# Kernel tuning notes

Hardware: AMD Instinct MI355X
Metric: run time of the kernel (lower is better)

Reference implementation:

```python
import jax, jax.numpy as jnp
import numpy as np

DIM = 128
N_HEADS = 4
HEAD_DIM = DIM // N_HEADS
EPS = 1e-5


def setup_inputs() -> dict:
    key = jax.random.key(0)
    ks = jax.random.split(key, 6)
    B, L, D = 1, 256, DIM
    s = 1.0 / np.sqrt(D)
    return {
        "z": jax.random.normal(ks[0], (B, L, L, D), dtype=jnp.float32),
        "ln_g": jnp.ones((D,), dtype=jnp.float32),
        "ln_b": jnp.zeros((D,), dtype=jnp.float32),
        "w_qkv": jax.random.normal(ks[1], (D, 3 * D), dtype=jnp.float32) * s,
        "b_qkv": jnp.zeros((3 * D,), dtype=jnp.float32),
        "w_proj": jax.random.normal(ks[2], (D, D), dtype=jnp.float32) * s,
        "b_proj": jnp.zeros((D,), dtype=jnp.float32),
    }


def reference(z, ln_g, ln_b, w_qkv, b_qkv, w_proj, b_proj):
    # z: (B, L1, L2, D); axis='row' -> attention along L2 for each (B, L1) row
    B, L1, L2, D = z.shape
    H, hd = N_HEADS, HEAD_DIM

    mu = jnp.mean(z, axis=-1, keepdims=True)
    var = jnp.mean(jnp.square(z - mu), axis=-1, keepdims=True)
    zn = (z - mu) * jax.lax.rsqrt(var + EPS) * ln_g + ln_b

    qkv = zn @ w_qkv + b_qkv                      # (B, L1, L2, 3D)
    qkv = qkv.reshape(B, L1, L2, 3, H, hd)
    q, k, v = qkv[..., 0, :, :], qkv[..., 1, :, :], qkv[..., 2, :, :]  # (B,L1,L2,H,hd)

    scale = 1.0 / jnp.sqrt(jnp.asarray(hd, dtype=z.dtype))
    attn = jnp.einsum("brqhd,brkhd->brhqk", q, k) * scale  # (B,L1,H,L2,L2)
    attn = jax.nn.softmax(attn, axis=-1)
    out = jnp.einsum("brhqk,brkhd->brqhd", attn, v)        # (B,L1,L2,H,hd)
    out = out.reshape(B, L1, L2, D)
    out = out @ w_proj + b_proj
    return z + out
```

## Files before the change

### kernel.cpp

```cpp
#include <hip/hip_runtime.h>
#include <hip/hip_bf16.h>


using ush = unsigned short;

__device__ __forceinline__ float bflo(unsigned int u) { return __uint_as_float(u << 16); }
__device__ __forceinline__ float bfhi(unsigned int u) { return __uint_as_float(u & 0xffff0000u); }
__device__ __forceinline__ float bf2f(unsigned short u) { return __uint_as_float(((unsigned int)u) << 16); }
__device__ __forceinline__ unsigned short f2bf(float f) {
    unsigned int i = __float_as_uint(f);
    i += 0x7fffu + ((i >> 16) & 1u);
    return (unsigned short)(i >> 16);
}
__device__ __forceinline__ void splitf(float x, unsigned short& h, unsigned short& l) {
    h = f2bf(x);
    l = f2bf(x - bf2f(h));
}

__device__ bool sniff_is_f32(const unsigned int* z) {
    int n = 0;
    for (int i = 0; i < 64; ++i) {
        float a = fabsf(bflo(z[i]));
        n += (int)(a > 1e4f) | (int)(a > 0.f && a < 1e-6f);
    }
    return n > 16;
}

template<bool F32> __device__ __forceinline__ float ldel(const void* p, int i) {
    if constexpr (F32) return ((const float*)p)[i];
    else               return bf2f(((const unsigned short*)p)[i]);
}
template<bool F32> __device__ __forceinline__ void ld8(const void* p, int i8, float* v) {
    if constexpr (F32) {
        const float4* q = (const float4*)p;
        float4 a = q[2 * i8], b = q[2 * i8 + 1];
        v[0]=a.x; v[1]=a.y; v[2]=a.z; v[3]=a.w; v[4]=b.x; v[5]=b.y; v[6]=b.z; v[7]=b.w;
    } else {
        uint4 u = ((const uint4*)p)[i8];
        const unsigned int* pu = (const unsigned int*)&u;
        #pragma unroll
        for (int j = 0; j < 4; ++j) { v[2*j] = bflo(pu[j]); v[2*j+1] = bfhi(pu[j]); }
    }
}
template<bool F32> __device__ __forceinline__ void st8(void* p, int i8, const float* v) {
    if constexpr (F32) {
        float4 a, b;
        a.x=v[0]; a.y=v[1]; a.z=v[2]; a.w=v[3];
        b.x=v[4]; b.y=v[5]; b.z=v[6]; b.w=v[7];
        ((float4*)p)[2 * i8] = a; ((float4*)p)[2 * i8 + 1] = b;
    } else {
        uint4 u; unsigned int* pu = (unsigned int*)&u;
        #pragma unroll
        for (int j = 0; j < 4; ++j)
            pu[j] = (unsigned int)f2bf(v[2*j]) | ((unsigned int)f2bf(v[2*j+1]) << 16);
        ((uint4*)p)[i8] = u;
    }
}
template<bool F32> __device__ __forceinline__ const void* elptr(const void* p, size_t off) {
    if constexpr (F32) return (const void*)((const float*)p + off);
    else               return (const void*)((const unsigned short*)p + off);
}
template<bool F32> __device__ __forceinline__ void* elptrw(void* p, size_t off) {
    if constexpr (F32) return (void*)((float*)p + off);
    else               return (void*)((unsigned short*)p + off);
}

using bf16x8 = __attribute__((ext_vector_type(8))) short;
using f32x4  = __attribute__((ext_vector_type(4))) float;

__device__ __forceinline__ f32x4 mfma16(bf16x8 a, bf16x8 b, f32x4 c) {
    return __builtin_amdgcn_mfma_f32_16x16x32_bf16(a, b, c, 0, 0, 0);
}

__device__ __forceinline__ int sw_off (int row, int k) {
    return row * 32 + ((((k >> 3) ^ (row >> 1)) & 3) << 3) + (k & 7);
}
__device__ __forceinline__ int sw_frag(int row, int g) {
    return row * 32 + (((g ^ (row >> 1)) & 3) << 3);
}
__device__ __forceinline__ int vt_off(int dim, int key) {
    return dim * 256 + (key ^ ((dim & 7) << 3));
}

#define WS_NEED 265216ull

template<bool F32>
__global__ __launch_bounds__(256) void prep_w(
    const void* __restrict__ z, const void* __restrict__ ln_g, const void* __restrict__ ln_b,
    const void* __restrict__ w_qkv, const void* __restrict__ b_qkv, const void* __restrict__ w_proj,
    ush* __restrict__ wqSH, ush* __restrict__ wqSL,
    ush* __restrict__ wpH, ush* __restrict__ wpL,
    float* __restrict__ biasG, float* __restrict__ csumG)
{
    if (sniff_is_f32((const unsigned int*)z) != F32) return;
    const int gid = blockIdx.x * 256 + threadIdx.x;
    const int NT  = 96 * 256;

    for (int e = gid; e < 49152; e += NT) {
        int kl = e & 31;
        int c  = (e >> 5) % 96;
        int hk = e / 3072;
        int h  = hk >> 2, kc = hk & 3;
        int k  = kc * 32 + kl;
        int gc = ((c >> 5) << 7) + (h << 5) + (c & 31);
        float wv = ldel<F32>(ln_g, k) * ldel<F32>(w_qkv, k * 384 + gc);
        ush hh, ll; splitf(wv, hh, ll);
        int o = hk * 3072 + sw_off(c, kl);
        wqSH[o] = hh; wqSL[o] = ll;
    }
    for (int e = gid; e < 16384; e += NT) {
        int c = e >> 7, k = e & 127;
        float v = ldel<F32>(w_proj, k * 128 + c);
        ush hh, ll; splitf(v, hh, ll);
        wpH[e] = hh; wpL[e] = ll;
    }
    if (gid < 384 * 64) {
        const int pair = gid >> 6;
        const int lane = gid & 63;
        const int h = pair / 96, c = pair % 96;
        const int gc = ((c >> 5) << 7) + (h << 5) + (c & 31);
        const float w0 = ldel<F32>(w_qkv, lane * 384 + gc);
        const float w1 = ldel<F32>(w_qkv, (lane + 64) * 384 + gc);
        float s  = ldel<F32>(ln_b, lane) * w0 + ldel<F32>(ln_b, lane + 64) * w1;
        float s2 = ldel<F32>(ln_g, lane) * w0 + ldel<F32>(ln_g, lane + 64) * w1;
        #pragma unroll
        for (int d = 1; d < 64; d <<= 1) { s += __shfl_xor(s, d); s2 += __shfl_xor(s2, d); }
        if (lane == 0) { biasG[pair] = ldel<F32>(b_qkv, gc) + s; csumG[pair] = s2; }
    }
}

template<bool F32>
__global__ __launch_bounds__(512, 2) void attn_mfma4(
    const void* __restrict__ z, const ush* __restrict__ wqSH, const ush* __restrict__ wqSL,
    const float* __restrict__ biasG, const float* __restrict__ csumG, void* __restrict__ out)
{
    if (sniff_is_f32((const unsigned int*)z) != F32) return;

    __shared__ __align__(16) unsigned char smem[57344];
    ush* znH  = (ush*)smem;
    ush* znL  = (ush*)(smem + 16384);
    ush* wtH  = (ush*)(smem + 32768);
    ush* wtL  = (ush*)(smem + 38912);
    ush* kHs  = znH;
    ush* kLs  = znL;
    ush* vtH  = (ush*)(smem + 32768);

    const int t    = threadIdx.x;
    const int lane = t & 63;
    const int w    = t >> 6;
    const int g    = lane >> 4;
    const int c16  = lane & 15;
    const int xcd  = blockIdx.x & 7;
    const int jj   = blockIdx.x >> 3;
    const int r    = (xcd << 5) | (jj >> 2);
    const int h    = jj & 3;
    ush* ps = (ush*)(smem + 49152) + (w << 9);

    const int rowl  = lane & 31;
    const int shalf = lane >> 5;
    const int srow  = (w << 5) | rowl;
    const void* zsrow = elptr<F32>(z, ((size_t)r * 256 + srow) << 7);

    float bv[6], cs[6];
    #pragma unroll
    for (int ct = 0; ct < 6; ++ct) {
        bv[ct] = biasG[h * 96 + ct * 16 + c16];
        cs[ct] = csumG[h * 96 + ct * 16 + c16];
    }

    f32x4 acc[2][6];
    #pragma unroll
    for (int qt = 0; qt < 2; ++qt)
        #pragma unroll
        for (int ct = 0; ct < 6; ++ct)
            #pragma unroll
            for (int rr = 0; rr < 4; ++rr) acc[qt][ct][rr] = 0.f;

    float sum = 0.f, sumsq = 0.f;

    #pragma unroll 1
    for (int kc = 0; kc < 4; ++kc) {
        if constexpr (!F32) {
            #pragma unroll
            for (int q8 = 0; q8 < 2; ++q8) {
                const int i8 = (shalf << 1) | q8;
                uint4 u = ((const uint4*)zsrow)[kc * 4 + i8];
                *(uint4*)&znH[sw_frag(srow, i8)] = u;
                const unsigned int* pu = (const unsigned int*)&u;
                #pragma unroll
                for (int j = 0; j < 4; ++j) {
                    float a = bflo(pu[j]), b = bfhi(pu[j]);
                    sum += a + b; sumsq += a * a + b * b;
                }
            }
        } else {
            float vv[8];
            #pragma unroll
            for (int q8 = 0; q8 < 2; ++q8) {
                const int i8 = (shalf << 1) | q8;
                ld8<F32>(zsrow, kc * 4 + i8, vv);
                union { ush s[8]; uint4 v4; } uh, ul;
                #pragma unroll
                for (int j = 0; j < 8; ++j) {
                    splitf(vv[j], uh.s[j], ul.s[j]);
                    sum += vv[j]; sumsq += vv[j] * vv[j];
                }
                int b2 = sw_frag(srow, i8);
                *(uint4*)&znH[b2] = uh.v4;
                *(uint4*)&znL[b2] = ul.v4;
            }
        }
        {
            const uint4* srcH = (const uint4*)(wqSH + (h * 4 + kc) * 3072);
            const uint4* srcL = (const uint4*)(wqSL + (h * 4 + kc) * 3072);
            #pragma unroll
            for (int i = t; i < 768; i += 512) {
                if (i < 384) ((uint4*)wtH)[i]       = srcH[i];
                else         ((uint4*)wtL)[i - 384] = srcL[i - 384];
            }
        }
        __syncthreads();

        bf16x8 bH[6], bL[6];
        #pragma unroll
        for (int ct = 0; ct < 6; ++ct) {
            int brow = ct * 16 + c16;
            bH[ct] = *(const bf16x8*)&wtH[sw_frag(brow, g)];
            bL[ct] = *(const bf16x8*)&wtL[sw_frag(brow, g)];
        }
        #pragma unroll
        for (int qt = 0; qt < 2; ++qt) {
            int arow = (w << 5) + (qt << 4) + c16;
            bf16x8 aHf = *(const bf16x8*)&znH[sw_frag(arow, g)];
            if constexpr (!F32) {
                #pragma unroll
                for (int ct = 0; ct < 6; ++ct) {
                    acc[qt][ct] = mfma16(aHf, bH[ct], acc[qt][ct]);
                    acc[qt][ct] = mfma16(aHf, bL[ct], acc[qt][ct]);
                }
            } else {
                bf16x8 aLf = *(const bf16x8*)&znL[sw_frag(arow, g)];
                #pragma unroll
                for (int ct = 0; ct < 6; ++ct) {
                    acc[qt][ct] = mfma16(aHf, bH[ct], acc[qt][ct]);
                    acc[qt][ct] = mfma16(aHf, bL[ct], acc[qt][ct]);
                    acc[qt][ct] = mfma16(aLf, bH[ct], acc[qt][ct]);
                }
            }
        }
        __syncthreads();
    }

    sum   += __shfl_xor(sum, 32);
    sumsq += __shfl_xor(sumsq, 32);

    const float mu   = sum * (1.f / 128.f);
    const float rsig = 1.0f / sqrtf(sumsq * (1.f / 128.f) - mu * mu + 1e-5f);
    const float nb   = -mu * rsig;

    float* pf = (float*)ps;
    pf[lane & 31] = rsig; pf[64 + (lane & 31)] = nb;
    __asm__ volatile("" ::: "memory");

    #pragma unroll
    for (int qt = 0; qt < 2; ++qt) {
        #pragma unroll
        for (int rr = 0; rr < 4; ++rr) {
            const int j = (qt << 4) + 4 * g + rr;
            const float rs = pf[j];
            const float nv = pf[64 + j];
            #pragma unroll
            for (int ct = 0; ct < 6; ++ct)
                acc[qt][ct][rr] = fmaf(rs, acc[qt][ct][rr], fmaf(nv, cs[ct], bv[ct]));
        }
    }
    __asm__ volatile("" ::: "memory");

    #pragma unroll
    for (int qt = 0; qt < 2; ++qt) {
        #pragma unroll
        for (int rr = 0; rr < 4; ++rr) {
            int key = (w << 5) + (qt << 4) + 4 * g + rr;
            ush hh, ll;
            splitf(acc[qt][2][rr], hh, ll);
            kHs[sw_off(key, c16)]      = hh; kLs[sw_off(key, c16)]      = ll;
            splitf(acc[qt][3][rr], hh, ll);
            kHs[sw_off(key, 16 + c16)] = hh; kLs[sw_off(key, 16 + c16)] = ll;
            vtH[vt_off(c16,      key)] = f2bf(acc[qt][4][rr]);
            vtH[vt_off(16 + c16, key)] = f2bf(acc[qt][5][rr]);
        }
    }

    const float SCALE = 0.17677669529663689f;
    bf16x8 qfH[2], qfL[2];
    #pragma unroll
    for (int qt = 0; qt < 2; ++qt) {
        #pragma unroll
        for (int rr = 0; rr < 4; ++rr) {
            int rw = 4 * g + rr;
            ps[sw_off(rw, c16)]      = f2bf(acc[qt][0][rr] * SCALE);
            ps[sw_off(rw, 16 + c16)] = f2bf(acc[qt][1][rr] * SCALE);
        }
        qfH[qt] = *(const bf16x8*)&ps[sw_frag(c16, g)];
        #pragma unroll
        for (int rr = 0; rr < 4; ++rr) {
            int rw = 4 * g + rr;
            float q0 = acc[qt][0][rr] * SCALE;
            float q1 = acc[qt][1][rr] * SCALE;
            ps[sw_off(rw, c16)]      = f2bf(q0 - bf2f(f2bf(q0)));
            ps[sw_off(rw, 16 + c16)] = f2bf(q1 - bf2f(f2bf(q1)));
        }
        qfL[qt] = *(const bf16x8*)&ps[sw_frag(c16, g)];
    }
    __syncthreads();

    float m[8], l[8];
    #pragma unroll
    for (int i = 0; i < 8; ++i) { m[i] = -3.0e38f; l[i] = 0.f; }
    f32x4 O[2][2];
    #pragma unroll
    for (int qt = 0; qt < 2; ++qt)
        #pragma unroll
        for (int dt = 0; dt < 2; ++dt)
            #pragma unroll
            for (int rr = 0; rr < 4; ++rr) O[qt][dt][rr] = 0.f;

    f32x4 zed; zed[0] = 0.f; zed[1] = 0.f; zed[2] = 0.f; zed[3] = 0.f;

    #pragma unroll 1
    for (int kb = 0; kb < 8; ++kb) {
        int key0 = kb * 32;
        bf16x8 kfH[2], kfL[2], vf[2];
        #pragma unroll
        for (int kt = 0; kt < 2; ++kt) {
            int krow = key0 + 16 * kt + c16;
            kfH[kt] = *(const bf16x8*)&kHs[sw_frag(krow, g)];
            kfL[kt] = *(const bf16x8*)&kLs[sw_frag(krow, g)];
        }
        #pragma unroll
        for (int dt = 0; dt < 2; ++dt)
            vf[dt] = *(const bf16x8*)&vtH[vt_off(16 * dt + c16, key0 + 8 * g)];

        #pragma unroll
        for (int qt = 0; qt < 2; ++qt) {
            f32x4 s0 = mfma16(qfH[qt], kfH[0], zed);
            s0 = mfma16(qfH[qt], kfL[0], s0);
            s0 = mfma16(qfL[qt], kfH[0], s0);
            f32x4 s1 = mfma16(qfH[qt], kfH[1], zed);
            s1 = mfma16(qfH[qt], kfL[1], s1);
            s1 = mfma16(qfL[qt], kfH[1], s1);

            #pragma unroll
            for (int rr = 0; rr < 4; ++rr) {
                float mx = fmaxf(s0[rr], s1[rr]);
                mx = fmaxf(mx, __shfl_xor(mx, 1));
                mx = fmaxf(mx, __shfl_xor(mx, 2));
                mx = fmaxf(mx, __shfl_xor(mx, 4));
                mx = fmaxf(mx, __shfl_xor(mx, 8));
                const int idx = qt * 4 + rr;
                float mo = m[idx];
                float mn = fmaxf(mo, mx);
                float al = __expf(fmaxf(mo - mn, -87.f));
                float p0 = __expf(s0[rr] - mn);
                float p1 = __expf(s1[rr] - mn);
                l[idx] = l[idx] * al + p0 + p1;
                m[idx] = mn;
                O[qt][0][rr] *= al;
                O[qt][1][rr] *= al;
                int rw = 4 * g + rr;
                ps[sw_off(rw, c16)]      = f2bf(p0);
                ps[sw_off(rw, 16 + c16)] = f2bf(p1);
            }
            bf16x8 pf2 = *(const bf16x8*)&ps[sw_frag(c16, g)];
            O[qt][0] = mfma16(pf2, vf[0], O[qt][0]);
            O[qt][1] = mfma16(pf2, vf[1], O[qt][1]);
        }
    }

    #pragma unroll
    for (int i = 0; i < 8; ++i) {
        float s = l[i];
        s += __shfl_xor(s, 1);
        s += __shfl_xor(s, 2);
        s += __shfl_xor(s, 4);
        s += __shfl_xor(s, 8);
        l[i] = s;
    }

    #pragma unroll
    for (int qt = 0; qt < 2; ++qt) {
        #pragma unroll
        for (int rr = 0; rr < 4; ++rr) {
            float rlv = 1.f / l[qt * 4 + rr];
            int grow = (r << 8) + (w << 5) + (qt << 4) + 4 * g + rr;
            size_t base = ((size_t)grow << 7) + (h << 5);
            if constexpr (F32) {
                float* po = (float*)out + base;
                po[c16]      = O[qt][0][rr] * rlv;
                po[16 + c16] = O[qt][1][rr] * rlv;
            } else {
                ush* po = (ush*)out + base;
                po[c16]      = f2bf(O[qt][0][rr] * rlv);
                po[16 + c16] = f2bf(O[qt][1][rr] * rlv);
            }
        }
    }
}

template<bool F32>
__global__ __launch_bounds__(256) void proj_mfma2(
    const void* __restrict__ z, const void* __restrict__ b_proj,
    const ush* __restrict__ wpH, const ush* __restrict__ wpL,
    void* __restrict__ out)
{
    if (sniff_is_f32((const unsigned int*)z) != F32) return;

    const int t    = threadIdx.x;
    const int lane = t & 63;
    const int w    = t >> 6;
    const int g    = lane >> 4;
    const int c16  = lane & 15;
    const int tok0 = blockIdx.x * 64 + w * 16;

    f32x4 acc[8];
    #pragma unroll
    for (int at = 0; at < 8; ++at)
        #pragma unroll
        for (int rr = 0; rr < 4; ++rr) acc[at][rr] = 0.f;

    #pragma unroll 1
    for (int kc = 0; kc < 4; ++kc) {
        const int token = tok0 + c16;
        float av[8];
        ld8<F32>(elptr<F32>((const void*)out, (size_t)token * 128 + kc * 32 + 8 * g), 0, av);
        union { ush s[8]; bf16x8 v; } hU, lU;
        #pragma unroll
        for (int j = 0; j < 8; ++j) splitf(av[j], hU.s[j], lU.s[j]);
        const bf16x8 btH = hU.v;
        const bf16x8 btL = lU.v;

        #pragma unroll
        for (int at = 0; at < 8; ++at) {
            const size_t wrow = (size_t)(at * 16 + c16) * 128 + kc * 32 + 8 * g;
            bf16x8 awH = *(const bf16x8*)&wpH[wrow];
            acc[at] = mfma16(awH, btH, acc[at]);
            if constexpr (F32) {
                bf16x8 awL = *(const bf16x8*)&wpL[wrow];
                acc[at] = mfma16(awH, btL, acc[at]);
                acc[at] = mfma16(awL, btH, acc[at]);
            }
        }
    }

    #pragma unroll
    for (int at = 0; at < 8; ++at) {
        const int c0 = at * 16 + 4 * g;
        float bp[4];
        #pragma unroll
        for (int rr = 0; rr < 4; ++rr) bp[rr] = ldel<F32>(b_proj, c0 + rr);
        const int n = tok0 + c16;
        const size_t ob = (size_t)n * 128 + c0;
        if constexpr (F32) {
            const float4 zv = *(const float4*)((const float*)z + ob);
            float4 o;
            o.x = acc[at][0] + bp[0] + zv.x;
            o.y = acc[at][1] + bp[1] + zv.y;
            o.z = acc[at][2] + bp[2] + zv.z;
            o.w = acc[at][3] + bp[3] + zv.w;
            *(float4*)((float*)out + ob) = o;
        } else {
            const uint2 zu = *(const uint2*)((const ush*)z + ob);
            float v0 = acc[at][0] + bp[0] + bflo(zu.x);
            float v1 = acc[at][1] + bp[1] + bfhi(zu.x);
            float v2 = acc[at][2] + bp[2] + bflo(zu.y);
            float v3 = acc[at][3] + bp[3] + bfhi(zu.y);
            uint2 u;
            u.x = (unsigned int)f2bf(v0) | ((unsigned int)f2bf(v1) << 16);
            u.y = (unsigned int)f2bf(v2) | ((unsigned int)f2bf(v3) << 16);
            *(uint2*)((ush*)out + ob) = u;
        }
    }
}

template<bool F32>
__global__ __launch_bounds__(256) void attn_mfma(
    const void* __restrict__ z, const void* __restrict__ ln_g, const void* __restrict__ ln_b,
    const void* __restrict__ w_qkv, const void* __restrict__ b_qkv, void* __restrict__ out)
{
    if (sniff_is_f32((const unsigned int*)z) != F32) return;

    __shared__ __align__(16) unsigned char smem[53248];
    ush* znH  = (ush*)smem;
    ush* znL  = (ush*)(smem + 16384);
    ush* wtH  = (ush*)(smem + 32768);
    ush* wtL  = (ush*)(smem + 38912);
    float* biasm = (float*)(smem + 45056);
    ush* kHs  = znH;
    ush* kLs  = znL;
    ush* vtH  = (ush*)(smem + 32768);

    const int t    = threadIdx.x;
    const int lane = t & 63;
    const int w    = t >> 6;
    const int g    = lane >> 4;
    const int c16  = lane & 15;
    const int r    = blockIdx.x >> 2;
    const int h    = blockIdx.x & 3;
    ush* ps = (ush*)(smem + 49152) + (w << 9);

    if (t < 96) {
        int gc = ((t >> 5) << 7) + (h << 5) + (t & 31);
        float b0 = 0.f, b1 = 0.f;
        #pragma unroll 8
        for (int k = 0; k < 128; k += 2) {
            b0 += ldel<F32>(ln_b, k)     * ldel<F32>(w_qkv, k * 384 + gc);
            b1 += ldel<F32>(ln_b, k + 1) * ldel<F32>(w_qkv, (k + 1) * 384 + gc);
        }
        biasm[t] = ldel<F32>(b_qkv, gc) + b0 + b1;
    }

    const void* zrow = elptr<F32>(z, ((size_t)r * 256 + t) << 7);
    float sum = 0.f, sumsq = 0.f;
    #pragma unroll 1
    for (int i = 0; i < 16; ++i) {
        float v[8]; ld8<F32>(zrow, i, v);
        #pragma unroll
        for (int j = 0; j < 8; ++j) { sum += v[j]; sumsq += v[j] * v[j]; }
    }
    const float mu   = sum * (1.f / 128.f);
    const float rsig = 1.0f / sqrtf(sumsq * (1.f / 128.f) - mu * mu + 1e-5f);
    const float nb   = -mu * rsig;

    __syncthreads();

    float bv[6];
    #pragma unroll
    for (int ct = 0; ct < 6; ++ct) bv[ct] = biasm[ct * 16 + c16];

    f32x4 acc[4][6];
    #pragma unroll
    for (int qt = 0; qt < 4; ++qt)
        #pragma unroll
        for (int ct = 0; ct < 6; ++ct)
            #pragma unroll
            for (int rr = 0; rr < 4; ++rr) acc[qt][ct][rr] = 0.f;

    #pragma unroll 1
    for (int kc = 0; kc < 4; ++kc) {
        {
            float vv[8];
            #pragma unroll
            for (int i8 = 0; i8 < 4; ++i8) {
                ld8<F32>(zrow, kc * 4 + i8, vv);
                union { ush s[8]; uint4 v4; } uh, ul;
                #pragma unroll
                for (int j = 0; j < 8; ++j) {
                    float zh = fmaf(vv[j], rsig, nb);
                    splitf(zh, uh.s[j], ul.s[j]);
                }
                int b2 = sw_frag(t, i8);
                *(uint4*)&znH[b2] = uh.v4;
                *(uint4*)&znL[b2] = ul.v4;
            }
        }
        for (int idx = t; idx < 3072; idx += 256) {
            int c  = idx % 96;
            int kl = idx / 96;
            int kk = kc * 32 + kl;
            int gc = ((c >> 5) << 7) + (h << 5) + (c & 31);
            float wv = ldel<F32>(ln_g, kk) * ldel<F32>(w_qkv, kk * 384 + gc);
            ush hh, ll; splitf(wv, hh, ll);
            int o = sw_off(c, kl);
            wtH[o] = hh; wtL[o] = ll;
        }
        __syncthreads();

        bf16x8 bH[6], bL[6];
        #pragma unroll
        for (int ct = 0; ct < 6; ++ct) {
            int brow = ct * 16 + c16;
            bH[ct] = *(const bf16x8*)&wtH[sw_frag(brow, g)];
            bL[ct] = *(const bf16x8*)&wtL[sw_frag(brow, g)];
        }
        #pragma unroll
        for (int qt = 0; qt < 4; ++qt) {
            int arow = (w << 6) + (qt << 4) + c16;
            bf16x8 aHf = *(const bf16x8*)&znH[sw_frag(arow, g)];
            bf16x8 aLf = *(const bf16x8*)&znL[sw_frag(arow, g)];
            #pragma unroll
            for (int ct = 0; ct < 6; ++ct) {
                acc[qt][ct] = mfma16(aHf, bH[ct], acc[qt][ct]);
                acc[qt][ct] = mfma16(aHf, bL[ct], acc[qt][ct]);
                acc[qt][ct] = mfma16(aLf, bH[ct], acc[qt][ct]);
            }
        }
        __syncthreads();
    }

    #pragma unroll
    for (int qt = 0; qt < 4; ++qt)
        #pragma unroll
        for (int ct = 0; ct < 6; ++ct)
            #pragma unroll
            for (int rr = 0; rr < 4; ++rr) acc[qt][ct][rr] += bv[ct];

    #pragma unroll
    for (int qt = 0; qt < 4; ++qt) {
        #pragma unroll
        for (int rr = 0; rr < 4; ++rr) {
            int key = (w << 6) + (qt << 4) + 4 * g + rr;
            ush hh, ll;
            splitf(acc[qt][2][rr], hh, ll);
            kHs[sw_off(key, c16)]      = hh; kLs[sw_off(key, c16)]      = ll;
            splitf(acc[qt][3][rr], hh, ll);
            kHs[sw_off(key, 16 + c16)] = hh; kLs[sw_off(key, 16 + c16)] = ll;
            vtH[vt_off(c16,      key)] = f2bf(acc[qt][4][rr]);
            vtH[vt_off(16 + c16, key)] = f2bf(acc[qt][5][rr]);
        }
    }

    const float SCALE = 0.17677669529663689f;
    bf16x8 qfH[4], qfL[4];
    #pragma unroll
    for (int qt = 0; qt < 4; ++qt) {
        #pragma unroll
        for (int rr = 0; rr < 4; ++rr) {
            int rw = 4 * g + rr;
            ps[sw_off(rw, c16)]      = f2bf(acc[qt][0][rr] * SCALE);
            ps[sw_off(rw, 16 + c16)] = f2bf(acc[qt][1][rr] * SCALE);
        }
        qfH[qt] = *(const bf16x8*)&ps[sw_frag(c16, g)];
        #pragma unroll
        for (int rr = 0; rr < 4; ++rr) {
            int rw = 4 * g + rr;
            float q0 = acc[qt][0][rr] * SCALE;
            float q1 = acc[qt][1][rr] * SCALE;
            ps[sw_off(rw, c16)]      = f2bf(q0 - bf2f(f2bf(q0)));
            ps[sw_off(rw, 16 + c16)] = f2bf(q1 - bf2f(f2bf(q1)));
        }
        qfL[qt] = *(const bf16x8*)&ps[sw_frag(c16, g)];
    }
    __syncthreads();

    float m[16], l[16];
    #pragma unroll
    for (int i = 0; i < 16; ++i) { m[i] = -3.0e38f; l[i] = 0.f; }
    f32x4 O[4][2];
    #pragma unroll
    for (int qt = 0; qt < 4; ++qt)
        #pragma unroll
        for (int dt = 0; dt < 2; ++dt)
            #pragma unroll
            for (int rr = 0; rr < 4; ++rr) O[qt][dt][rr] = 0.f;

    f32x4 zed; zed[0] = 0.f; zed[1] = 0.f; zed[2] = 0.f; zed[3] = 0.f;

    #pragma unroll 1
    for (int kb = 0; kb < 8; ++kb) {
        int key0 = kb * 32;
        bf16x8 kfH[2], kfL[2], vf[2];
        #pragma unroll
        for (int kt = 0; kt < 2; ++kt) {
            int krow = key0 + 16 * kt + c16;
            kfH[kt] = *(const bf16x8*)&kHs[sw_frag(krow, g)];
            kfL[kt] = *(const bf16x8*)&kLs[sw_frag(krow, g)];
        }
        #pragma unroll
        for (int dt = 0; dt < 2; ++dt)
            vf[dt] = *(const bf16x8*)&vtH[vt_off(16 * dt + c16, key0 + 8 * g)];

        #pragma unroll
        for (int qt = 0; qt < 4; ++qt) {
            f32x4 s0 = mfma16(qfH[qt], kfH[0], zed);
            s0 = mfma16(qfH[qt], kfL[0], s0);
            s0 = mfma16(qfL[qt], kfH[0], s0);
            f32x4 s1 = mfma16(qfH[qt], kfH[1], zed);
            s1 = mfma16(qfH[qt], kfL[1], s1);
            s1 = mfma16(qfL[qt], kfH[1], s1);

            #pragma unroll
            for (int rr = 0; rr < 4; ++rr) {
                float mx = fmaxf(s0[rr], s1[rr]);
                mx = fmaxf(mx, __shfl_xor(mx, 1));
                mx = fmaxf(mx, __shfl_xor(mx, 2));
                mx = fmaxf(mx, __shfl_xor(mx, 4));
                mx = fmaxf(mx, __shfl_xor(mx, 8));
                const int idx = qt * 4 + rr;
                float mo = m[idx];
                float mn = fmaxf(mo, mx);
                float al = __expf(fmaxf(mo - mn, -87.f));
                float p0 = __expf(s0[rr] - mn);
                float p1 = __expf(s1[rr] - mn);
                l[idx] = l[idx] * al + p0 + p1;
                m[idx] = mn;
                O[qt][0][rr] *= al;
                O[qt][1][rr] *= al;
                int rw = 4 * g + rr;
                ps[sw_off(rw, c16)]      = f2bf(p0);
                ps[sw_off(rw, 16 + c16)] = f2bf(p1);
            }
            bf16x8 pf = *(const bf16x8*)&ps[sw_frag(c16, g)];
            O[qt][0] = mfma16(pf, vf[0], O[qt][0]);
            O[qt][1] = mfma16(pf, vf[1], O[qt][1]);
        }
    }

    #pragma unroll
    for (int i = 0; i < 16; ++i) {
        float s = l[i];
        s += __shfl_xor(s, 1);
        s += __shfl_xor(s, 2);
        s += __shfl_xor(s, 4);
        s += __shfl_xor(s, 8);
        l[i] = s;
    }

    #pragma unroll
    for (int qt = 0; qt < 4; ++qt) {
        #pragma unroll
        for (int rr = 0; rr < 4; ++rr) {
            float rlv = 1.f / l[qt * 4 + rr];
            int grow = (r << 8) + (w << 6) + (qt << 4) + 4 * g + rr;
            size_t base = ((size_t)grow << 7) + (h << 5);
            if constexpr (F32) {
                float* po = (float*)out + base;
                po[c16]      = O[qt][0][rr] * rlv;
                po[16 + c16] = O[qt][1][rr] * rlv;
            } else {
                ush* po = (ush*)out + base;
                po[c16]      = f2bf(O[qt][0][rr] * rlv);
                po[16 + c16] = f2bf(O[qt][1][rr] * rlv);
            }
        }
    }
}

template<bool F32>
__global__ __launch_bounds__(256) void proj_res(
    const void* __restrict__ z, const void* __restrict__ w_proj, const void* __restrict__ b_proj,
    void* __restrict__ out)
{
    if (sniff_is_f32((const unsigned int*)z) != F32) return;

    __shared__ unsigned int wu[8192];
    __shared__ float aT[128][20];

    const int t = threadIdx.x;
    const size_t row0 = (size_t)blockIdx.x * 16;

    if constexpr (!F32) {
        for (int idx = t; idx < 8192; idx += 256)
            wu[idx] = ((const unsigned int*)w_proj)[idx];
    }

    {
        const int rr = t >> 4;
        const int i8 = t & 15;
        float v[8];
        ld8<F32>(elptr<F32>((const void*)out, (row0 + rr) * 128), i8, v);
        #pragma unroll
        for (int j = 0; j < 8; ++j) aT[(i8 << 3) + j][rr] = v[j];
    }
    __syncthreads();

    const int c = t & 127;
    const int half = t >> 7;
    float acc8[8];
    const float bp = ldel<F32>(b_proj, c);
    #pragma unroll
    for (int rr = 0; rr < 8; ++rr) acc8[rr] = bp;

    #pragma unroll 1
    for (int k = 0; k < 128; ++k) {
        float wk;
        if constexpr (F32) {
            wk = ((const float*)w_proj)[k * 128 + c];
        } else {
            unsigned int u = wu[(k << 6) + (c >> 1)];
            wk = (c & 1) ? bfhi(u) : bflo(u);
        }
        const float4 a0 = *(const float4*)&aT[k][half * 8];
        const float4 a1 = *(const float4*)&aT[k][half * 8 + 4];
        acc8[0] = fmaf(a0.x, wk, acc8[0]);
        acc8[1] = fmaf(a0.y, wk, acc8[1]);
        acc8[2] = fmaf(a0.z, wk, acc8[2]);
        acc8[3] = fmaf(a0.w, wk, acc8[3]);
        acc8[4] = fmaf(a1.x, wk, acc8[4]);
        acc8[5] = fmaf(a1.y, wk, acc8[5]);
        acc8[6] = fmaf(a1.z, wk, acc8[6]);
        acc8[7] = fmaf(a1.w, wk, acc8[7]);
    }
    __syncthreads();
    float* ot = (float*)aT;
    #pragma unroll
    for (int rr = 0; rr < 8; ++rr)
        ot[(half * 8 + rr) * 128 + c] = acc8[rr];
    __syncthreads();

    {
        const int rr = t >> 4;
        const int i8 = t & 15;
        float zv[8], v[8];
        ld8<F32>(elptr<F32>(z, (row0 + rr) * 128), i8, zv);
        const float* po = &ot[rr * 128 + (i8 << 3)];
        #pragma unroll
        for (int j = 0; j < 8; ++j) v[j] = po[j] + zv[j];
        st8<F32>(elptrw<F32>(out, (row0 + rr) * 128), i8, v);
    }
}

extern "C" void kernel_launch(void* const* d_in, const int* in_sizes, int n_in,
                              void* d_out, int out_size, void* d_ws, size_t ws_size,
                              hipStream_t stream) {
    const void* z      = d_in[0];
    const void* ln_g   = d_in[1];
    const void* ln_b   = d_in[2];
    const void* w_qkv  = d_in[3];
    const void* b_qkv  = d_in[4];
    const void* w_proj = d_in[5];
    const void* b_proj = d_in[6];
    void* out = d_out;

    if (ws_size >= WS_NEED && d_ws != nullptr) {
        unsigned char* W = (unsigned char*)d_ws;
        ush*   wqSH  = (ush*)(W + 0);
        ush*   wqSL  = (ush*)(W + 98304);
        ush*   wpH   = (ush*)(W + 196608);
        ush*   wpL   = (ush*)(W + 229376);
        float* biasG = (float*)(W + 262144);
        float* csumG = (float*)(W + 263680);

        prep_w<false><<<96, 256, 0, stream>>>(z, ln_g, ln_b, w_qkv, b_qkv, w_proj, wqSH, wqSL, wpH, wpL, biasG, csumG);
        prep_w<true ><<<96, 256, 0, stream>>>(z, ln_g, ln_b, w_qkv, b_qkv, w_proj, wqSH, wqSL, wpH, wpL, biasG, csumG);
        attn_mfma4<false><<<1024, 512, 0, stream>>>(z, wqSH, wqSL, biasG, csumG, out);
        attn_mfma4<true ><<<1024, 512, 0, stream>>>(z, wqSH, wqSL, biasG, csumG, out);
        proj_mfma2<false><<<1024, 256, 0, stream>>>(z, b_proj, wpH, wpL, out);
        proj_mfma2<true ><<<1024, 256, 0, stream>>>(z, b_proj, wpH, wpL, out);
    } else {
        attn_mfma<false><<<1024, 256, 0, stream>>>(z, ln_g, ln_b, w_qkv, b_qkv, out);
        attn_mfma<true ><<<1024, 256, 0, stream>>>(z, ln_g, ln_b, w_qkv, b_qkv, out);
        proj_res<false><<<4096, 256, 0, stream>>>(z, w_proj, b_proj, out);
        proj_res<true ><<<4096, 256, 0, stream>>>(z, w_proj, b_proj, out);
    }
}
```

Measured before the change: 247.1 us.

## Transpose attention MFMA operands so each lane owns one query row

Swaps the A/B operands of the QK^T and PV MFMAs, so the score tile comes out transposed and each lane holds four keys of a single query. The softmax max and sum then reduce within a lane plus two cross-lane shuffles, replacing four shuffles per row. The running max/sum state shrinks from 8 to 2 registers per lane. P is packed into 8-byte LDS writes and outputs go out as vectorized float4/uint2 stores instead of scalar stores. The risk is that the new swizzled write offsets for P must line up exactly with the fragment read layout.

```diff
diff --git a/kernel.cpp b/kernel.cpp
--- a/kernel.cpp
+++ b/kernel.cpp
@@ -130,7 +130,7 @@
 }
 
 template<bool F32>
-__global__ __launch_bounds__(512, 2) void attn_mfma4(
+__global__ __launch_bounds__(512, 2) void attn_mfma5(
     const void* __restrict__ z, const ush* __restrict__ wqSH, const ush* __restrict__ wqSL,
     const float* __restrict__ biasG, const float* __restrict__ csumG, void* __restrict__ out)
 {
@@ -258,8 +258,8 @@
     const float rsig = 1.0f / sqrtf(sumsq * (1.f / 128.f) - mu * mu + 1e-5f);
     const float nb   = -mu * rsig;
 
-    float* pf = (float*)ps;
-    pf[lane & 31] = rsig; pf[64 + (lane & 31)] = nb;
+    float* pf0 = (float*)ps;
+    pf0[lane & 31] = rsig; pf0[64 + (lane & 31)] = nb;
     __asm__ volatile("" ::: "memory");
 
     #pragma unroll
@@ -267,8 +267,8 @@
         #pragma unroll
         for (int rr = 0; rr < 4; ++rr) {
             const int j = (qt << 4) + 4 * g + rr;
-            const float rs = pf[j];
-            const float nv = pf[64 + j];
+            const float rs = pf0[j];
+            const float nv = pf0[64 + j];
             #pragma unroll
             for (int ct = 0; ct < 6; ++ct)
                 acc[qt][ct][rr] = fmaf(rs, acc[qt][ct][rr], fmaf(nv, cs[ct], bv[ct]));
@@ -314,9 +314,9 @@
     }
     __syncthreads();
 
-    float m[8], l[8];
-    #pragma unroll
-    for (int i = 0; i < 8; ++i) { m[i] = -3.0e38f; l[i] = 0.f; }
+    float m[2], l[2];
+    #pragma unroll
+    for (int i = 0; i < 2; ++i) { m[i] = -3.0e38f; l[i] = 0.f; }
     f32x4 O[2][2];
     #pragma unroll
     for (int qt = 0; qt < 2; ++qt)
@@ -326,6 +326,9 @@
             for (int rr = 0; rr < 4; ++rr) O[qt][dt][rr] = 0.f;
 
     f32x4 zed; zed[0] = 0.f; zed[1] = 0.f; zed[2] = 0.f; zed[3] = 0.f;
+
+    const int wr0 = c16 * 32 + (((( (g >> 1)    ) ^ (c16 >> 1)) & 3) << 3) + ((g & 1) << 2);
+    const int wr1 = c16 * 32 + (((( (g >> 1) + 2) ^ (c16 >> 1)) & 3) << 3) + ((g & 1) << 2);
 
     #pragma unroll 1
     for (int kb = 0; kb < 8; ++kb) {
@@ -343,65 +346,71 @@
 
         #pragma unroll
         for (int qt = 0; qt < 2; ++qt) {
-            f32x4 s0 = mfma16(qfH[qt], kfH[0], zed);
-            s0 = mfma16(qfH[qt], kfL[0], s0);
-            s0 = mfma16(qfL[qt], kfH[0], s0);
-            f32x4 s1 = mfma16(qfH[qt], kfH[1], zed);
-            s1 = mfma16(qfH[qt], kfL[1], s1);
-            s1 = mfma16(qfL[qt], kfH[1], s1);
-
+            f32x4 s0 = mfma16(kfH[0], qfH[qt], zed);
+            s0 = mfma16(kfH[0], qfL[qt], s0);
+            s0 = mfma16(kfL[0], qfH[qt], s0);
+            f32x4 s1 = mfma16(kfH[1], qfH[qt], zed);
+            s1 = mfma16(kfH[1], qfL[qt], s1);
+            s1 = mfma16(kfL[1], qfH[qt], s1);
+
+            float pmax = fmaxf(fmaxf(fmaxf(s0[0], s0[1]), fmaxf(s0[2], s0[3])),
+                               fmaxf(fmaxf(s1[0], s1[1]), fmaxf(s1[2], s1[3])));
+            pmax = fmaxf(pmax, __shfl_xor(pmax, 16));
+            pmax = fmaxf(pmax, __shfl_xor(pmax, 32));
+
+            const float mo = m[qt];
+            const float mn = fmaxf(mo, pmax);
+            const float al = __expf(fmaxf(mo - mn, -87.f));
+            float p0[4], p1[4], psum = 0.f;
             #pragma unroll
             for (int rr = 0; rr < 4; ++rr) {
-                float mx = fmaxf(s0[rr], s1[rr]);
-                mx = fmaxf(mx, __shfl_xor(mx, 1));
-                mx = fmaxf(mx, __shfl_xor(mx, 2));
-                mx = fmaxf(mx, __shfl_xor(mx, 4));
-                mx = fmaxf(mx, __shfl_xor(mx, 8));
-                const int idx = qt * 4 + rr;
-                float mo = m[idx];
-                float mn = fmaxf(mo, mx);
-                float al = __expf(fmaxf(mo - mn, -87.f));
-                float p0 = __expf(s0[rr] - mn);
-                float p1 = __expf(s1[rr] - mn);
-                l[idx] = l[idx] * al + p0 + p1;
-                m[idx] = mn;
-                O[qt][0][rr] *= al;
-                O[qt][1][rr] *= al;
-                int rw = 4 * g + rr;
-                ps[sw_off(rw, c16)]      = f2bf(p0);
-                ps[sw_off(rw, 16 + c16)] = f2bf(p1);
-            }
-            bf16x8 pf2 = *(const bf16x8*)&ps[sw_frag(c16, g)];
-            O[qt][0] = mfma16(pf2, vf[0], O[qt][0]);
-            O[qt][1] = mfma16(pf2, vf[1], O[qt][1]);
-        }
-    }
-
-    #pragma unroll
-    for (int i = 0; i < 8; ++i) {
-        float s = l[i];
-        s += __shfl_xor(s, 1);
-        s += __shfl_xor(s, 2);
-        s += __shfl_xor(s, 4);
-        s += __shfl_xor(s, 8);
-        l[i] = s;
+                p0[rr] = __expf(s0[rr] - mn);
+                p1[rr] = __expf(s1[rr] - mn);
+                psum += p0[rr] + p1[rr];
+            }
+            l[qt] = l[qt] * al + psum;
+            m[qt] = mn;
+            #pragma unroll
+            for (int rr = 0; rr < 4; ++rr) { O[qt][0][rr] *= al; O[qt][1][rr] *= al; }
+
+            uint2 u01, u23;
+            u01.x = (unsigned int)f2bf(p0[0]) | ((unsigned int)f2bf(p0[1]) << 16);
+            u01.y = (unsigned int)f2bf(p0[2]) | ((unsigned int)f2bf(p0[3]) << 16);
+            u23.x = (unsigned int)f2bf(p1[0]) | ((unsigned int)f2bf(p1[1]) << 16);
+            u23.y = (unsigned int)f2bf(p1[2]) | ((unsigned int)f2bf(p1[3]) << 16);
+            *(uint2*)&ps[wr0] = u01;
+            *(uint2*)&ps[wr1] = u23;
+            __asm__ volatile("" ::: "memory");
+            bf16x8 pfr = *(const bf16x8*)&ps[sw_frag(c16, g)];
+            __asm__ volatile("" ::: "memory");
+
+            O[qt][0] = mfma16(vf[0], pfr, O[qt][0]);
+            O[qt][1] = mfma16(vf[1], pfr, O[qt][1]);
+        }
     }
 
     #pragma unroll
     for (int qt = 0; qt < 2; ++qt) {
-        #pragma unroll
-        for (int rr = 0; rr < 4; ++rr) {
-            float rlv = 1.f / l[qt * 4 + rr];
-            int grow = (r << 8) + (w << 5) + (qt << 4) + 4 * g + rr;
-            size_t base = ((size_t)grow << 7) + (h << 5);
+        float s = l[qt];
+        s += __shfl_xor(s, 16);
+        s += __shfl_xor(s, 32);
+        const float rlv = 1.f / s;
+        const int token = (r << 8) + (w << 5) + (qt << 4) + c16;
+        #pragma unroll
+        for (int dt = 0; dt < 2; ++dt) {
+            const size_t ob = ((size_t)token << 7) + (h << 5) + (dt << 4) + 4 * g;
             if constexpr (F32) {
-                float* po = (float*)out + base;
-                po[c16]      = O[qt][0][rr] * rlv;
-                po[16 + c16] = O[qt][1][rr] * rlv;
+                float4 o;
+                o.x = O[qt][dt][0] * rlv;
+                o.y = O[qt][dt][1] * rlv;
+                o.z = O[qt][dt][2] * rlv;
+                o.w = O[qt][dt][3] * rlv;
+                *(float4*)((float*)out + ob) = o;
             } else {
-                ush* po = (ush*)out + base;
-                po[c16]      = f2bf(O[qt][0][rr] * rlv);
-                po[16 + c16] = f2bf(O[qt][1][rr] * rlv);
+                uint2 u;
+                u.x = (unsigned int)f2bf(O[qt][dt][0] * rlv) | ((unsigned int)f2bf(O[qt][dt][1] * rlv) << 16);
+                u.y = (unsigned int)f2bf(O[qt][dt][2] * rlv) | ((unsigned int)f2bf(O[qt][dt][3] * rlv) << 16);
+                *(uint2*)((ush*)out + ob) = u;
             }
         }
     }
@@ -832,8 +841,8 @@
 
         prep_w<false><<<96, 256, 0, stream>>>(z, ln_g, ln_b, w_qkv, b_qkv, w_proj, wqSH, wqSL, wpH, wpL, biasG, csumG);
         prep_w<true ><<<96, 256, 0, stream>>>(z, ln_g, ln_b, w_qkv, b_qkv, w_proj, wqSH, wqSL, wpH, wpL, biasG, csumG);
-        attn_mfma4<false><<<1024, 512, 0, stream>>>(z, wqSH, wqSL, biasG, csumG, out);
-        attn_mfma4<true ><<<1024, 512, 0, stream>>>(z, wqSH, wqSL, biasG, csumG, out);
+        attn_mfma5<false><<<1024, 512, 0, stream>>>(z, wqSH, wqSL, biasG, csumG, out);
+        attn_mfma5<true ><<<1024, 512, 0, stream>>>(z, wqSH, wqSL, biasG, csumG, out);
         proj_mfma2<false><<<1024, 256, 0, stream>>>(z, b_proj, wpH, wpL, out);
         proj_mfma2<true ><<<1024, 256, 0, stream>>>(z, b_proj, wpH, wpL, out);
     } else {
```

After: 232.5 us. -5.9%, faster.
